# Kernel optimization log

Measured on AMD Instinct MI355X. Metric: run time of the kernel, lower is better.

## Reference

```python
import jax, jax.numpy as jnp
import numpy as np

N = 2_000_000           # agents
T = 10                  # timesteps
G_HOUSEHOLD = 800_000   # groups per edge type
G_COMPANY = 20_000
G_SCHOOL = 65_000
TAU = 0.1               # gumbel-softmax temperature (GradABM-JUNE default)


def setup_inputs() -> dict:
    key = jax.random.key(0)
    ks = jax.random.split(key, 6)
    # pre-sampled standard Gumbel noise for the differentiable Bernoulli sampling
    u = jax.random.uniform(ks[0], (T, 2, N), minval=1e-9, maxval=1.0)
    gumbel = (-jnp.log(-jnp.log(u))).astype(jnp.float32)
    return {
        "beta_parameters": jnp.array([0.3, 0.2, 0.4], dtype=jnp.float32),
        "transmissions": 0.1 * jax.random.uniform(ks[1], (N,), dtype=jnp.float32),
        "susceptibilities": jnp.ones((N,), dtype=jnp.float32),
        "gumbel": gumbel,
        "g_household": jax.random.randint(ks[2], (N,), 0, G_HOUSEHOLD),
        "g_company": jax.random.randint(ks[3], (N,), 0, G_COMPANY),
        "g_school": jax.random.randint(ks[4], (N,), 0, G_SCHOOL),
        "n_timesteps": T,
    }


def _infection_step(betas, transm, susc, gumbel_t, group_ids, group_sizes):
    """One InfectionPassing forward + gumbel-softmax sampling."""
    trans_susc = jnp.zeros_like(transm)
    for beta, gids, G in zip(betas, group_ids, group_sizes):
        # group sizes -> contact probability (constant wrt params)
        people = jax.ops.segment_sum(jnp.ones_like(transm), gids, num_segments=G)
        p_contact = jax.lax.stop_gradient(jnp.minimum(1.0 / (people - 1.0), 1.0))
        # agent -> group scatter-add of transmissions, weighted by beta * p_contact
        cum_trans = beta * p_contact * jax.ops.segment_sum(transm, gids, num_segments=G)
        # group -> agent gather, weighted by susceptibility
        trans_susc = trans_susc + cum_trans[gids] * susc
    not_infected = jnp.exp(-trans_susc)
    # hard (straight-through) gumbel-softmax Bernoulli sample, class 1 = infected
    logits = jnp.log(jnp.clip(jnp.stack([not_infected, 1.0 - not_infected]), 1e-15))  # [2, N]
    y = jax.nn.softmax((logits + gumbel_t) / TAU, axis=0)
    hard = jax.nn.one_hot(jnp.argmax(y, axis=0), 2, axis=0, dtype=y.dtype)
    sample = hard + y - jax.lax.stop_gradient(y)
    return sample[1]


def reference(beta_parameters, transmissions, susceptibilities, gumbel,
              g_household, g_company, g_school, n_timesteps):
    group_ids = (g_household, g_company, g_school)
    group_sizes = (G_HOUSEHOLD, G_COMPANY, G_SCHOOL)
    betas = (beta_parameters[0], beta_parameters[1], beta_parameters[2])

    def scan_fn(carry, gumbel_t):
        transm, susc = carry
        new_inf = _infection_step(betas, transm, susc, gumbel_t, group_ids, group_sizes)
        return (transm + 0.2 * new_inf, susc - new_inf), new_inf

    _, ret = jax.lax.scan(scan_fn, (transmissions, susceptibilities), gumbel[:n_timesteps])
    return ret  # [T, N] stacked new_infected per timestep (vstack equivalent)
```

## Files before the change

### kernel.cpp

```cpp
#include <hip/hip_runtime.h>

#define GHN 800000
#define GCN 20000
#define GSN 65000
#define GT  885000
#define TSTEPS 10

#define FIXD   17592186044416.0
#define INVFIX (1.0 / 17592186044416.0)
#define DELTA  3518437208883ULL
#define CUNIT  (1ULL << 51)
#define SMASK  (CUNIT - 1ULL)

typedef float vf4 __attribute__((ext_vector_type(4)));

__global__ void init_kernel(const float* __restrict__ transm_in,
                            const int* __restrict__ gh,
                            const int* __restrict__ gc,
                            const int* __restrict__ gs,
                            unsigned long long* __restrict__ buf,
                            int n) {
    int i = blockIdx.x * blockDim.x + threadIdx.x;
    if (i >= n) return;
    float t = transm_in[i];
    unsigned long long e =
        (unsigned long long)((double)t * FIXD + 0.5) + CUNIT;
    atomicAdd(&buf[gh[i]], e);
    atomicAdd(&buf[GHN + gc[i]], e);
    atomicAdd(&buf[GHN + GCN + gs[i]], e);
}

__global__ void combine_kernel(const float* __restrict__ betas,
                               const unsigned long long* __restrict__ buf,
                               float* __restrict__ cur) {
    int g4 = (blockIdx.x * blockDim.x + threadIdx.x) * 4;
    if (g4 >= GT) return;
    ulonglong2 v01 = *(const ulonglong2*)(buf + g4);
    ulonglong2 v23 = *(const ulonglong2*)(buf + g4 + 2);
    float beta = (g4 < GHN) ? betas[0] : (g4 < GHN + GCN) ? betas[1] : betas[2];
    unsigned long long vv[4] = {v01.x, v01.y, v23.x, v23.y};
    vf4 o;
#pragma unroll
    for (int k = 0; k < 4; ++k) {
        unsigned long long v = vv[k];
        float people = (float)(v >> 51);
        float p = fminf(1.0f / (people - 1.0f), 1.0f);
        float sum = (float)((double)(long long)(v & SMASK) * INVFIX);
        o[k] = (beta * p) * sum;
    }
    *(vf4*)(cur + g4) = o;
}

template <bool LAST>
__global__ __launch_bounds__(256)
void step_kernel(const float* __restrict__ gum_t,
                 const int* __restrict__ gh,
                 const int* __restrict__ gc,
                 const int* __restrict__ gs,
                 const float* __restrict__ cur,
                 unsigned long long* __restrict__ buf,
                 float* __restrict__ susc,
                 float* __restrict__ out_t,
                 int n) {
    int base = (blockIdx.x * blockDim.x + threadIdx.x) * 4;
    if (base >= n) return;

    int4 a4 = *(const int4*)(gh + base);
    int4 b4 = *(const int4*)(gc + base);
    int4 c4 = *(const int4*)(gs + base);
    float4 s4 = *(const float4*)(susc + base);
    vf4 g0 = __builtin_nontemporal_load((const vf4*)(gum_t + base));
    vf4 g1 = __builtin_nontemporal_load((const vf4*)(gum_t + n + base));

    int ga[4] = {a4.x, a4.y, a4.z, a4.w};
    int gb[4] = {GHN + b4.x, GHN + b4.y, GHN + b4.z, GHN + b4.w};
    int gcx[4] = {GHN + GCN + c4.x, GHN + GCN + c4.y,
                  GHN + GCN + c4.z, GHN + GCN + c4.w};
    float sv[4] = {s4.x, s4.y, s4.z, s4.w};

    float ca[4], cb[4], cc[4];
#pragma unroll
    for (int j = 0; j < 4; ++j) {
        ca[j] = cur[ga[j]];
        cb[j] = cur[gb[j]];
        cc[j] = cur[gcx[j]];
    }

    vf4 og = {0.0f, 0.0f, 0.0f, 0.0f};
#pragma unroll
    for (int j = 0; j < 4; ++j) {
        if (sv[j] != 0.0f) {
            float ts = ca[j];
            ts += cb[j];
            ts += cc[j];
            float ni = expf(-ts);
            float l0 = logf(fmaxf(ni, 1e-15f));
            float l1 = logf(fmaxf(1.0f - ni, 1e-15f));
            float z0 = (l0 + g0[j]) / 0.1f;
            float z1 = (l1 + g1[j]) / 0.1f;
            if (z1 > z0) {
                og[j] = 1.0f;
                sv[j] = sv[j] - 1.0f;
                if (!LAST) {
                    atomicAdd(&buf[ga[j]],  DELTA);
                    atomicAdd(&buf[gb[j]],  DELTA);
                    atomicAdd(&buf[gcx[j]], DELTA);
                }
            }
        }
    }

    *(float4*)(susc + base) = make_float4(sv[0], sv[1], sv[2], sv[3]);
    __builtin_nontemporal_store(og, (vf4*)(out_t + base));
}

extern "C" void kernel_launch(void* const* d_in, const int* in_sizes, int n_in,
                              void* d_out, int out_size, void* d_ws, size_t ws_size,
                              hipStream_t stream) {
    const float* betas     = (const float*)d_in[0];
    const float* transm_in = (const float*)d_in[1];
    float*       susc      = (float*)d_in[2];
    const float* gumbel    = (const float*)d_in[3];
    const int*   gh        = (const int*)d_in[4];
    const int*   gc        = (const int*)d_in[5];
    const int*   gs        = (const int*)d_in[6];
    const int    n         = in_sizes[1];
    float*       out       = (float*)d_out;

    unsigned long long* buf = (unsigned long long*)d_ws;
    float* cur = (float*)((char*)d_ws + (size_t)GT * 8);

    const int blk = 256;
    const int grid_init = (n + blk - 1) / blk;
    const int grid_comb = (GT / 4 + blk - 1) / blk;
    const int grid_step = (n / 4 + blk - 1) / blk;

    hipMemsetAsync(buf, 0, (size_t)GT * 8, stream);

    init_kernel<<<grid_init, blk, 0, stream>>>(transm_in, gh, gc, gs, buf, n);

    for (int t = 0; t < TSTEPS; ++t) {
        const float* gum_t = gumbel + (size_t)2 * t * n;
        float* out_t = out + (size_t)t * n;

        combine_kernel<<<grid_comb, blk, 0, stream>>>(betas, buf, cur);

        if (t == TSTEPS - 1) {
            step_kernel<true><<<grid_step, blk, 0, stream>>>(
                gum_t, gh, gc, gs, cur, buf, susc, out_t, n);
        } else {
            step_kernel<false><<<grid_step, blk, 0, stream>>>(
                gum_t, gh, gc, gs, cur, buf, susc, out_t, n);
        }
    }
}
```

Baseline: 975.3 us.

## Replace susceptibility floats with per-octet live bitmask and process 8 agents per thread

Susceptibility is tracked as an 8-bit live mask per group of 8 agents instead of a float array, built once in the init kernel. Step kernels handle 8 agents per thread, skip all loads for fully infected octets, and write the mask only when it changes. This cuts per-step memory traffic for susceptibility and can skip gather work. It relies on susceptibility values being exactly 0 or 1 and on n being a multiple of 8.

Measured after the change: 977.5 us. Within noise of the previous version (+0.2%).

```diff
diff --git a/kernel.cpp b/kernel.cpp
--- a/kernel.cpp
+++ b/kernel.cpp
@@ -12,22 +12,49 @@
 #define CUNIT  (1ULL << 51)
 #define SMASK  (CUNIT - 1ULL)
 
+#define APT 8
+
 typedef float vf4 __attribute__((ext_vector_type(4)));
 
 __global__ void init_kernel(const float* __restrict__ transm_in,
+                            const float* __restrict__ susc_in,
                             const int* __restrict__ gh,
                             const int* __restrict__ gc,
                             const int* __restrict__ gs,
                             unsigned long long* __restrict__ buf,
+                            unsigned char* __restrict__ live,
                             int n) {
-    int i = blockIdx.x * blockDim.x + threadIdx.x;
-    if (i >= n) return;
-    float t = transm_in[i];
-    unsigned long long e =
-        (unsigned long long)((double)t * FIXD + 0.5) + CUNIT;
-    atomicAdd(&buf[gh[i]], e);
-    atomicAdd(&buf[GHN + gc[i]], e);
-    atomicAdd(&buf[GHN + GCN + gs[i]], e);
+    int tid = blockIdx.x * blockDim.x + threadIdx.x;
+    int base = tid * APT;
+    if (base >= n) return;
+
+    float tr[APT], su[APT];
+    int ga[APT], gb[APT], gcx[APT];
+    *(float4*)&tr[0] = *(const float4*)(transm_in + base);
+    *(float4*)&tr[4] = *(const float4*)(transm_in + base + 4);
+    *(float4*)&su[0] = *(const float4*)(susc_in + base);
+    *(float4*)&su[4] = *(const float4*)(susc_in + base + 4);
+    *(int4*)&ga[0]  = *(const int4*)(gh + base);
+    *(int4*)&ga[4]  = *(const int4*)(gh + base + 4);
+    *(int4*)&gb[0]  = *(const int4*)(gc + base);
+    *(int4*)&gb[4]  = *(const int4*)(gc + base + 4);
+    *(int4*)&gcx[0] = *(const int4*)(gs + base);
+    *(int4*)&gcx[4] = *(const int4*)(gs + base + 4);
+
+    unsigned int m = 0;
+#pragma unroll
+    for (int j = 0; j < APT; ++j)
+        m |= (su[j] != 0.0f ? 1u : 0u) << j;
+    live[tid] = (unsigned char)m;
+
+#pragma unroll
+    for (int j = 0; j < APT; ++j) {
+        unsigned long long e =
+            (unsigned long long)((double)tr[j] * FIXD + 0.5) + CUNIT;
+        atomicAdd(&buf[ga[j]], e);
+        atomicAdd(&buf[GHN + gb[j]], e);
+        atomicAdd(&buf[GHN + GCN + gcx[j]], e);
+    }
 }
 
 __global__ void combine_kernel(const float* __restrict__ betas,
@@ -52,55 +79,73 @@
 }
 
 template <bool LAST>
-__global__ __launch_bounds__(256)
-void step_kernel(const float* __restrict__ gum_t,
-                 const int* __restrict__ gh,
-                 const int* __restrict__ gc,
-                 const int* __restrict__ gs,
-                 const float* __restrict__ cur,
-                 unsigned long long* __restrict__ buf,
-                 float* __restrict__ susc,
-                 float* __restrict__ out_t,
-                 int n) {
-    int base = (blockIdx.x * blockDim.x + threadIdx.x) * 4;
+__global__ void step_kernel(const float* __restrict__ gum_t,
+                            const int* __restrict__ gh,
+                            const int* __restrict__ gc,
+                            const int* __restrict__ gs,
+                            const float* __restrict__ cur,
+                            unsigned long long* __restrict__ buf,
+                            unsigned char* __restrict__ live,
+                            float* __restrict__ out_t,
+                            int n) {
+    int tid = blockIdx.x * blockDim.x + threadIdx.x;
+    int base = tid * APT;
     if (base >= n) return;
 
-    int4 a4 = *(const int4*)(gh + base);
-    int4 b4 = *(const int4*)(gc + base);
-    int4 c4 = *(const int4*)(gs + base);
-    float4 s4 = *(const float4*)(susc + base);
-    vf4 g0 = __builtin_nontemporal_load((const vf4*)(gum_t + base));
-    vf4 g1 = __builtin_nontemporal_load((const vf4*)(gum_t + n + base));
-
-    int ga[4] = {a4.x, a4.y, a4.z, a4.w};
-    int gb[4] = {GHN + b4.x, GHN + b4.y, GHN + b4.z, GHN + b4.w};
-    int gcx[4] = {GHN + GCN + c4.x, GHN + GCN + c4.y,
-                  GHN + GCN + c4.z, GHN + GCN + c4.w};
-    float sv[4] = {s4.x, s4.y, s4.z, s4.w};
-
-    float ca[4], cb[4], cc[4];
-#pragma unroll
-    for (int j = 0; j < 4; ++j) {
+    vf4 zero = {0.0f, 0.0f, 0.0f, 0.0f};
+    unsigned int m = live[tid];
+    if (m == 0) {
+        __builtin_nontemporal_store(zero, (vf4*)(out_t + base));
+        __builtin_nontemporal_store(zero, (vf4*)(out_t + base + 4));
+        return;
+    }
+
+    int ga[APT], gb[APT], gcx[APT];
+    *(int4*)&ga[0]  = *(const int4*)(gh + base);
+    *(int4*)&ga[4]  = *(const int4*)(gh + base + 4);
+    *(int4*)&gb[0]  = *(const int4*)(gc + base);
+    *(int4*)&gb[4]  = *(const int4*)(gc + base + 4);
+    *(int4*)&gcx[0] = *(const int4*)(gs + base);
+    *(int4*)&gcx[4] = *(const int4*)(gs + base + 4);
+#pragma unroll
+    for (int j = 0; j < APT; ++j) {
+        gb[j]  += GHN;
+        gcx[j] += GHN + GCN;
+    }
+
+    float g0a[APT], g1a[APT];
+    *(vf4*)&g0a[0] = __builtin_nontemporal_load((const vf4*)(gum_t + base));
+    *(vf4*)&g0a[4] = __builtin_nontemporal_load((const vf4*)(gum_t + base + 4));
+    *(vf4*)&g1a[0] = __builtin_nontemporal_load((const vf4*)(gum_t + n + base));
+    *(vf4*)&g1a[4] = __builtin_nontemporal_load((const vf4*)(gum_t + n + base + 4));
+
+    float ca[APT], cb[APT], cc[APT];
+#pragma unroll
+    for (int j = 0; j < APT; ++j) {
         ca[j] = cur[ga[j]];
         cb[j] = cur[gb[j]];
         cc[j] = cur[gcx[j]];
     }
 
-    vf4 og = {0.0f, 0.0f, 0.0f, 0.0f};
-#pragma unroll
-    for (int j = 0; j < 4; ++j) {
-        if (sv[j] != 0.0f) {
+    float og[APT];
+#pragma unroll
+    for (int j = 0; j < APT; ++j) og[j] = 0.0f;
+
+    const unsigned int m0 = m;
+#pragma unroll
+    for (int j = 0; j < APT; ++j) {
+        if (m & (1u << j)) {
             float ts = ca[j];
             ts += cb[j];
             ts += cc[j];
             float ni = expf(-ts);
             float l0 = logf(fmaxf(ni, 1e-15f));
             float l1 = logf(fmaxf(1.0f - ni, 1e-15f));
-            float z0 = (l0 + g0[j]) / 0.1f;
-            float z1 = (l1 + g1[j]) / 0.1f;
+            float z0 = (l0 + g0a[j]) / 0.1f;
+            float z1 = (l1 + g1a[j]) / 0.1f;
             if (z1 > z0) {
                 og[j] = 1.0f;
-                sv[j] = sv[j] - 1.0f;
+                m &= ~(1u << j);
                 if (!LAST) {
                     atomicAdd(&buf[ga[j]],  DELTA);
                     atomicAdd(&buf[gb[j]],  DELTA);
@@ -110,8 +155,9 @@
         }
     }
 
-    *(float4*)(susc + base) = make_float4(sv[0], sv[1], sv[2], sv[3]);
-    __builtin_nontemporal_store(og, (vf4*)(out_t + base));
+    if (m != m0) live[tid] = (unsigned char)m;
+    __builtin_nontemporal_store(*(vf4*)&og[0], (vf4*)(out_t + base));
+    __builtin_nontemporal_store(*(vf4*)&og[4], (vf4*)(out_t + base + 4));
 }
 
 extern "C" void kernel_launch(void* const* d_in, const int* in_sizes, int n_in,
@@ -119,7 +165,7 @@
                               hipStream_t stream) {
     const float* betas     = (const float*)d_in[0];
     const float* transm_in = (const float*)d_in[1];
-    float*       susc      = (float*)d_in[2];
+    const float* susc_in   = (const float*)d_in[2];
     const float* gumbel    = (const float*)d_in[3];
     const int*   gh        = (const int*)d_in[4];
     const int*   gc        = (const int*)d_in[5];
@@ -129,15 +175,16 @@
 
     unsigned long long* buf = (unsigned long long*)d_ws;
     float* cur = (float*)((char*)d_ws + (size_t)GT * 8);
+    unsigned char* live = (unsigned char*)((char*)d_ws + (size_t)GT * 12);
 
     const int blk = 256;
-    const int grid_init = (n + blk - 1) / blk;
+    const int grid_oct  = (n / APT + blk - 1) / blk;
     const int grid_comb = (GT / 4 + blk - 1) / blk;
-    const int grid_step = (n / 4 + blk - 1) / blk;
 
     hipMemsetAsync(buf, 0, (size_t)GT * 8, stream);
 
-    init_kernel<<<grid_init, blk, 0, stream>>>(transm_in, gh, gc, gs, buf, n);
+    init_kernel<<<grid_oct, blk, 0, stream>>>(transm_in, susc_in,
+                                              gh, gc, gs, buf, live, n);
 
     for (int t = 0; t < TSTEPS; ++t) {
         const float* gum_t = gumbel + (size_t)2 * t * n;
@@ -146,11 +193,11 @@
         combine_kernel<<<grid_comb, blk, 0, stream>>>(betas, buf, cur);
 
         if (t == TSTEPS - 1) {
-            step_kernel<true><<<grid_step, blk, 0, stream>>>(
-                gum_t, gh, gc, gs, cur, buf, susc, out_t, n);
+            step_kernel<true><<<grid_oct, blk, 0, stream>>>(
+                gum_t, gh, gc, gs, cur, buf, live, out_t, n);
         } else {
-            step_kernel<false><<<grid_step, blk, 0, stream>>>(
-                gum_t, gh, gc, gs, cur, buf, susc, out_t, n);
+            step_kernel<false><<<grid_oct, blk, 0, stream>>>(
+                gum_t, gh, gc, gs, cur, buf, live, out_t, n);
         }
     }
 }
```
